# Kernel optimization log

Measured on AMD Instinct MI355X. Metric: run time of the kernel, lower is better.

## Reference

```python
import jax, jax.numpy as jnp
import numpy as np

N_WAY = 64
EPS = 1e-5  # torch LayerNorm default


def _layernorm(x, g, b):
    mu = jnp.mean(x, axis=-1, keepdims=True)
    var = jnp.mean(jnp.square(x - mu), axis=-1, keepdims=True)
    return (x - mu) * jax.lax.rsqrt(var + EPS) * g + b


def _backbone(x, params):
    (W1, b1, g1, be1, W2, b2, g2, be2, W3, b3, g3, be3, W4, b4) = params
    h = jax.nn.relu(_layernorm(x @ W1.T + b1, g1, be1))
    h = jax.nn.relu(_layernorm(h @ W2.T + b2, g2, be2))
    h = jax.nn.relu(_layernorm(h @ W3.T + b3, g3, be3))
    return h @ W4.T + b4


def setup_inputs() -> dict:
    key = jax.random.key(0)
    ks = jax.random.split(key, 20)
    d = {}
    d["support_features"] = jax.random.normal(ks[0], (32768, 768), jnp.float32)
    d["support_labels"] = jax.random.randint(ks[1], (32768,), 0, N_WAY, jnp.int64)
    d["query_features"] = jax.random.normal(ks[2], (65536, 768), jnp.float32)
    dims = [(512, 768), (512, 512), (128, 512), (32, 128)]
    ki = 3
    for i, (dout, din) in enumerate(dims, start=1):
        scale = 1.0 / np.sqrt(din)
        d[f"W{i}"] = jax.random.uniform(ks[ki], (dout, din), jnp.float32, -scale, scale); ki += 1
        d[f"b{i}"] = jax.random.uniform(ks[ki], (dout,), jnp.float32, -scale, scale); ki += 1
        if i < 4:
            d[f"g{i}"] = jnp.ones((dout,), jnp.float32)
            d[f"be{i}"] = jnp.zeros((dout,), jnp.float32)
    return d


def reference(support_features, support_labels, query_features,
              W1, b1, g1, be1, W2, b2, g2, be2, W3, b3, g3, be3, W4, b4):
    params = (W1, b1, g1, be1, W2, b2, g2, be2, W3, b3, g3, be3, W4, b4)
    z_support = _backbone(support_features, params)   # [Ns, 32]
    z_query = _backbone(query_features, params)       # [Nq, 32]
    # segment-mean prototypes (replaces per-class nonzero+mean loop)
    sums = jax.ops.segment_sum(z_support, support_labels, num_segments=N_WAY)
    counts = jax.ops.segment_sum(jnp.ones((z_support.shape[0],), z_support.dtype),
                                 support_labels, num_segments=N_WAY)
    z_proto = sums / jnp.maximum(counts, 1.0)[:, None]  # [n_way, 32]
    # -cdist (euclidean)
    sq = (jnp.sum(z_query * z_query, axis=1)[:, None]
          + jnp.sum(z_proto * z_proto, axis=1)[None, :]
          - 2.0 * z_query @ z_proto.T)
    return -jnp.sqrt(jnp.maximum(sq, 0.0))  # [Nq, n_way]
```

## Files before the change

kernel.cpp:

```cpp
#include <hip/hip_runtime.h>

typedef unsigned short u16;
typedef short bf16x8 __attribute__((ext_vector_type(8)));
typedef float f32x16 __attribute__((ext_vector_type(16)));
typedef unsigned short u16x4v __attribute__((ext_vector_type(4)));
typedef unsigned short u16x8v __attribute__((ext_vector_type(8)));

#define LN_EPS 1e-5f

__device__ __forceinline__ u16 f2bf(float v) {
    unsigned x = __float_as_uint(v);
    x += 0x7fffu + ((x >> 16) & 1u);
    return (u16)(x >> 16);
}
__device__ __forceinline__ float bf2f(u16 u) {
    return __uint_as_float(((unsigned)u) << 16);
}

#define GLD16(gp, lp) __builtin_amdgcn_global_load_lds( \
    (const __attribute__((address_space(1))) void*)(gp), \
    (__attribute__((address_space(3))) void*)(lp), 16, 0, 0)

__global__ __launch_bounds__(256)
void swizzle_split(const float* __restrict__ src, u16* __restrict__ hi,
                   u16* __restrict__ lo, int R, int DIN)
{
    __shared__ __align__(16) u16 SH[2][24][17][8];
    const int tid  = threadIdx.x;
    const int row0 = blockIdx.x * 16;
    const int QK   = DIN / 16;
    const int kq0  = QK * blockIdx.y;
    const int NKC  = DIN / 32;

    const int slots = 16 * QK;
    for (int s = tid; s < slots; s += 256) {
        int row = s / QK, kq = s % QK;
        float4 v = *(const float4*)(src + (long)(row0 + row) * DIN + (long)(kq0 + kq) * 4);
        int kc = kq >> 1, jh = (kq & 1) * 4;
        float vv[4] = {v.x, v.y, v.z, v.w};
        u16x4v h, l;
#pragma unroll
        for (int j = 0; j < 4; ++j) {
            u16 hb = f2bf(vv[j]);
            h[j] = hb;
            l[j] = f2bf(vv[j] - bf2f(hb));
        }
        *(u16x4v*)(&SH[0][kc][row][jh]) = h;
        *(u16x4v*)(&SH[1][kc][row][jh]) = l;
    }
    __syncthreads();
    const int chunks = NKC * 16;
    for (int s = tid; s < chunks; s += 256) {
        int row = s & 15, kc = s >> 4;
        long o = ((long)(kq0 / 2 + kc) * R + row0 + row) * 8;
        *(u16x8v*)(hi + o) = *(const u16x8v*)(&SH[0][kc][row][0]);
        *(u16x8v*)(lo + o) = *(const u16x8v*)(&SH[1][kc][row][0]);
    }
}

template<int DOUT, bool OUT_SPLIT, int NT>
__device__ __forceinline__ void ln_epilogue(
    f32x16 (&acc)[2][NT], float (&lnp)[4][64][2],
    const float* __restrict__ bias, const float* __restrict__ gam,
    const float* __restrict__ bet,
    u16* __restrict__ Yh, u16* __restrict__ Yl, float* __restrict__ Yf,
    long row0, int NR, int wv, int l31, int hh)
{
    float gg[NT], bb[NT], bev[NT];
#pragma unroll
    for (int u = 0; u < NT; ++u) {
        int c = wv * (DOUT / 4) + u * 32 + l31;
        bb[u] = bias[c]; gg[u] = gam[c]; bev[u] = bet[c];
    }
#pragma unroll
    for (int t = 0; t < 2; ++t)
#pragma unroll
        for (int r = 0; r < 16; ++r) {
            float s1 = 0.f, s2 = 0.f;
#pragma unroll
            for (int u = 0; u < NT; ++u) {
                float v = acc[t][u][r] + bb[u];
                acc[t][u][r] = v;
                s1 += v; s2 += v * v;
            }
#pragma unroll
            for (int off = 1; off < 32; off <<= 1) {
                s1 += __shfl_xor(s1, off, 64);
                s2 += __shfl_xor(s2, off, 64);
            }
            int row = t * 32 + (r & 3) + 8 * (r >> 2) + 4 * hh;
            if (l31 == r) { lnp[wv][row][0] = s1; lnp[wv][row][1] = s2; }
        }
    __syncthreads();
#pragma unroll
    for (int t = 0; t < 2; ++t)
#pragma unroll
        for (int r = 0; r < 16; ++r) {
            int row = t * 32 + (r & 3) + 8 * (r >> 2) + 4 * hh;
            float s1 = lnp[0][row][0] + lnp[1][row][0] + lnp[2][row][0] + lnp[3][row][0];
            float s2 = lnp[0][row][1] + lnp[1][row][1] + lnp[2][row][1] + lnp[3][row][1];
            float mean = s1 * (1.f / DOUT);
            float inv  = rsqrtf(s2 * (1.f / DOUT) - mean * mean + LN_EPS);
            long gr = row0 + row;
#pragma unroll
            for (int u = 0; u < NT; ++u) {
                int c = wv * (DOUT / 4) + u * 32 + l31;
                float v = (acc[t][u][r] - mean) * inv * gg[u] + bev[u];
                v = fmaxf(v, 0.f);
                if (OUT_SPLIT) {
                    u16 hv = f2bf(v);
                    long o = ((long)(c >> 3) * NR + gr) * 8 + (c & 7);
                    Yh[o] = hv;
                    Yl[o] = f2bf(v - bf2f(hv));
                } else {
                    Yf[gr * DOUT + c] = v;
                }
            }
        }
}

template<int DOUT>
__global__ __launch_bounds__(256, 2)
void mfma_layer1(const float* __restrict__ X,
                 const u16* __restrict__ Wh, const u16* __restrict__ Wl,
                 const float* __restrict__ bias, const float* __restrict__ gam,
                 const float* __restrict__ bet,
                 u16* __restrict__ Yh, u16* __restrict__ Yl,
                 int DIN, int NR, long rbase)
{
    constexpr int NT = DOUT / 128;
    __shared__ __align__(16) u16 AL[2][4][2][2][520];
    __shared__ float lnp[4][64][2];

    const int tid  = threadIdx.x;
    const int lane = tid & 63, wv = tid >> 6;
    const int l31  = lane & 31, hh = lane >> 5;
    const long lrow0 = (long)blockIdx.x * 64;
    const long row0  = rbase + lrow0;

    const int srow  = wv * 16 + (lane >> 2);
    const int kpart = lane & 3;
    const float* xp = X + (lrow0 + srow) * DIN + kpart * 16;

    f32x16 acc[2][NT];
#pragma unroll
    for (int t = 0; t < 2; ++t)
#pragma unroll
        for (int u = 0; u < NT; ++u)
#pragma unroll
            for (int e = 0; e < 16; ++e) acc[t][u][e] = 0.f;

    const int nslab = DIN / 64;

    auto stage = [&](const float* p, int buf) {
#pragma unroll
        for (int c = 0; c < 2; ++c) {
            float4 v0 = *(const float4*)(p + c * 8);
            float4 v1 = *(const float4*)(p + c * 8 + 4);
            float f[8] = {v0.x, v0.y, v0.z, v0.w, v1.x, v1.y, v1.z, v1.w};
            u16x8v h, l;
#pragma unroll
            for (int j = 0; j < 8; ++j) {
                u16 hb = f2bf(f[j]);
                h[j] = hb;
                l[j] = f2bf(f[j] - bf2f(hb));
            }
            *(u16x8v*)(&AL[buf][kpart][0][c][srow * 8]) = h;
            *(u16x8v*)(&AL[buf][kpart][1][c][srow * 8]) = l;
        }
    };

    stage(xp, 0);
    for (int sl = 0; sl < nslab; ++sl) {
        __syncthreads();
        const int cb = sl & 1;
        if (sl + 1 < nslab) stage(xp + (sl + 1) * 64, cb ^ 1);
#pragma unroll
        for (int s = 0; s < 4; ++s) {
            const int ks = sl * 4 + s;
            bf16x8 wf[NT][2], af[2][2];
#pragma unroll
            for (int u = 0; u < NT; ++u) {
                long wo = ((long)(2 * ks + hh) * DOUT + wv * (DOUT / 4) + u * 32 + l31) * 8;
                wf[u][0] = *(const bf16x8*)(Wh + wo);
                wf[u][1] = *(const bf16x8*)(Wl + wo);
            }
#pragma unroll
            for (int t = 0; t < 2; ++t) {
                af[t][0] = *(const bf16x8*)(&AL[cb][s][0][hh][(t * 32 + l31) * 8]);
                af[t][1] = *(const bf16x8*)(&AL[cb][s][1][hh][(t * 32 + l31) * 8]);
            }
#pragma unroll
            for (int t = 0; t < 2; ++t)
#pragma unroll
                for (int u = 0; u < NT; ++u) {
                    acc[t][u] = __builtin_amdgcn_mfma_f32_32x32x16_bf16(af[t][0], wf[u][0], acc[t][u], 0, 0, 0);
                    acc[t][u] = __builtin_amdgcn_mfma_f32_32x32x16_bf16(af[t][0], wf[u][1], acc[t][u], 0, 0, 0);
                    acc[t][u] = __builtin_amdgcn_mfma_f32_32x32x16_bf16(af[t][1], wf[u][0], acc[t][u], 0, 0, 0);
                }
        }
    }

    ln_epilogue<DOUT, true, NT>(acc, lnp, bias, gam, bet, Yh, Yl, nullptr,
                                row0, NR, wv, l31, hh);
}

template<int DOUT, bool OUT_SPLIT>
__global__ __launch_bounds__(256, 2)
void mfma_layer(const u16* __restrict__ Ah, const u16* __restrict__ Al,
                const u16* __restrict__ Wh, const u16* __restrict__ Wl,
                const float* __restrict__ bias, const float* __restrict__ gam,
                const float* __restrict__ bet,
                u16* __restrict__ Yh, u16* __restrict__ Yl,
                float* __restrict__ Yf, int DIN, int NR)
{
    constexpr int NT = DOUT / 128;
    __shared__ __align__(16) u16 AL[2][4][2][2][64 * 8];
    __shared__ float lnp[4][64][2];

    const int tid  = threadIdx.x;
    const int lane = tid & 63, wv = tid >> 6;
    const int l31  = lane & 31, hh = lane >> 5;
    const long row0 = (long)blockIdx.x * 64;

    const u16* gpA[4];
    const long stA = (long)8 * NR * 8;
#pragma unroll
    for (int t = 0; t < 4; ++t) {
        int p = t & 1, c = t >> 1;
        const u16* base = p ? Al : Ah;
        gpA[t] = base + ((long)(2 * wv + c) * NR + row0 + lane) * 8;
    }

    f32x16 acc[2][NT];
#pragma unroll
    for (int t = 0; t < 2; ++t)
#pragma unroll
        for (int u = 0; u < NT; ++u)
#pragma unroll
            for (int e = 0; e < 16; ++e) acc[t][u][e] = 0.f;

    const int nslab = DIN / 64;
#pragma unroll
    for (int t = 0; t < 4; ++t) {
        GLD16(gpA[t], &AL[0][wv][t & 1][t >> 1][0]);
        gpA[t] += stA;
    }

    for (int sl = 0; sl < nslab; ++sl) {
        __syncthreads();
        const int cb = sl & 1;
        if (sl + 1 < nslab) {
#pragma unroll
            for (int t = 0; t < 4; ++t) {
                GLD16(gpA[t], &AL[cb ^ 1][wv][t & 1][t >> 1][0]);
                gpA[t] += stA;
            }
        }
#pragma unroll
        for (int s = 0; s < 4; ++s) {
            const int ks = sl * 4 + s;
            bf16x8 wf[NT][2], af[2][2];
#pragma unroll
            for (int u = 0; u < NT; ++u) {
                long wo = ((long)(2 * ks + hh) * DOUT + wv * (DOUT / 4) + u * 32 + l31) * 8;
                wf[u][0] = *(const bf16x8*)(Wh + wo);
                wf[u][1] = *(const bf16x8*)(Wl + wo);
            }
#pragma unroll
            for (int t = 0; t < 2; ++t) {
                af[t][0] = *(const bf16x8*)(&AL[cb][s][0][hh][(t * 32 + l31) * 8]);
                af[t][1] = *(const bf16x8*)(&AL[cb][s][1][hh][(t * 32 + l31) * 8]);
            }
#pragma unroll
            for (int t = 0; t < 2; ++t)
#pragma unroll
                for (int u = 0; u < NT; ++u) {
                    acc[t][u] = __builtin_amdgcn_mfma_f32_32x32x16_bf16(af[t][0], wf[u][0], acc[t][u], 0, 0, 0);
                    acc[t][u] = __builtin_amdgcn_mfma_f32_32x32x16_bf16(af[t][0], wf[u][1], acc[t][u], 0, 0, 0);
                    acc[t][u] = __builtin_amdgcn_mfma_f32_32x32x16_bf16(af[t][1], wf[u][0], acc[t][u], 0, 0, 0);
                }
        }
    }

    ln_epilogue<DOUT, OUT_SPLIT, NT>(acc, lnp, bias, gam, bet, Yh, Yl, Yf,
                                     row0, NR, wv, l31, hh);
}

__global__ __launch_bounds__(256)
void layer4_k(const float* __restrict__ H, const float* __restrict__ W4,
              const float* __restrict__ b4, float* __restrict__ Z)
{
    __shared__ float Ws[32 * 128];
    __shared__ float bs[32];
    const int tid = threadIdx.x;
    for (int idx = tid; idx < 4096; idx += 256) Ws[idx] = W4[idx];
    if (tid < 32) bs[tid] = b4[tid];
    __syncthreads();

    long r = (long)blockIdx.x * 256 + tid;
    float acc[32];
#pragma unroll
    for (int c = 0; c < 32; ++c) acc[c] = 0.f;
    for (int k = 0; k < 128; k += 4) {
        float4 x = *(const float4*)(H + r * 128 + k);
#pragma unroll
        for (int c = 0; c < 32; ++c) {
            acc[c] = fmaf(x.x, Ws[c * 128 + k + 0], acc[c]);
            acc[c] = fmaf(x.y, Ws[c * 128 + k + 1], acc[c]);
            acc[c] = fmaf(x.z, Ws[c * 128 + k + 2], acc[c]);
            acc[c] = fmaf(x.w, Ws[c * 128 + k + 3], acc[c]);
        }
    }
#pragma unroll
    for (int c = 0; c < 32; ++c) Z[r * 32 + c] = acc[c] + bs[c];
}

__global__ __launch_bounds__(256)
void proto_k(const float* __restrict__ Zs, const int* __restrict__ lab,
             float* __restrict__ P)
{
    const int c = blockIdx.x;
    const int tid = threadIdx.x, lane = tid & 63, wv = tid >> 6;
    float acc[32];
#pragma unroll
    for (int d = 0; d < 32; ++d) acc[d] = 0.f;
    float cnt = 0.f;
    for (int i = tid; i < 32768; i += 256) {
        if (lab[i] == c) {
            cnt += 1.f;
#pragma unroll
            for (int d = 0; d < 32; ++d) acc[d] += Zs[(long)i * 32 + d];
        }
    }
    __shared__ float wsum[4][32];
    __shared__ float wcnt[4];
#pragma unroll
    for (int d = 0; d < 32; ++d) {
        float v = acc[d];
        for (int off = 32; off > 0; off >>= 1) v += __shfl_xor(v, off, 64);
        if (lane == 0) wsum[wv][d] = v;
    }
    {
        float v = cnt;
        for (int off = 32; off > 0; off >>= 1) v += __shfl_xor(v, off, 64);
        if (lane == 0) wcnt[wv] = v;
    }
    __syncthreads();
    if (tid < 32) {
        float s  = wsum[0][tid] + wsum[1][tid] + wsum[2][tid] + wsum[3][tid];
        float cn = wcnt[0] + wcnt[1] + wcnt[2] + wcnt[3];
        P[c * 32 + tid] = s / fmaxf(cn, 1.f);
    }
}

__global__ __launch_bounds__(256)
void dist_k(const float* __restrict__ Zq, const float* __restrict__ P,
            float* __restrict__ O)
{
    __shared__ float ps[64 * 32];
    __shared__ float pn[64];
    const int tid = threadIdx.x;
    for (int idx = tid; idx < 2048; idx += 256) ps[idx] = P[idx];
    __syncthreads();
    if (tid < 64) {
        float s = 0.f;
        for (int d = 0; d < 32; ++d) { float v = ps[tid * 32 + d]; s += v * v; }
        pn[tid] = s;
    }
    __syncthreads();

    long q = (long)blockIdx.x * 256 + tid;
    float zr[32];
#pragma unroll
    for (int d = 0; d < 32; d += 4) {
        float4 v = *(const float4*)(Zq + q * 32 + d);
        zr[d] = v.x; zr[d + 1] = v.y; zr[d + 2] = v.z; zr[d + 3] = v.w;
    }
    float zz = 0.f;
#pragma unroll
    for (int d = 0; d < 32; ++d) zz += zr[d] * zr[d];
    for (int p = 0; p < 64; ++p) {
        float dot = 0.f;
#pragma unroll
        for (int d = 0; d < 32; ++d) dot = fmaf(zr[d], ps[p * 32 + d], dot);
        float sq = zz + pn[p] - 2.f * dot;
        O[q * 64 + p] = -sqrtf(fmaxf(sq, 0.f));
    }
}

extern "C" void kernel_launch(void* const* d_in, const int* in_sizes, int n_in,
                              void* d_out, int out_size, void* d_ws, size_t ws_size,
                              hipStream_t stream)
{
    const float* supp = (const float*)d_in[0];
    const int*   lab  = (const int*)  d_in[1];
    const float* qry  = (const float*)d_in[2];
    const float* W1 = (const float*)d_in[3];  const float* b1 = (const float*)d_in[4];
    const float* g1 = (const float*)d_in[5];  const float* be1= (const float*)d_in[6];
    const float* W2 = (const float*)d_in[7];  const float* b2 = (const float*)d_in[8];
    const float* g2 = (const float*)d_in[9];  const float* be2= (const float*)d_in[10];
    const float* W3 = (const float*)d_in[11]; const float* b3 = (const float*)d_in[12];
    const float* g3 = (const float*)d_in[13]; const float* be3= (const float*)d_in[14];
    const float* W4 = (const float*)d_in[15]; const float* b4 = (const float*)d_in[16];
    float* out = (float*)d_out;

    const long NTOT = 98304, NS = 32768, NQ = 65536;
    const int  NR = (int)NTOT;

    char* wsp = (char*)d_ws;
    size_t off = 0;
    auto take = [&](size_t bytes) {
        char* p = wsp + off;
        off += (bytes + 255) & ~(size_t)255;
        return (void*)p;
    };

    float* zAll  = (float*)take((size_t)NTOT * 32 * 4);
    float* proto = (float*)take(2048 * 4);
    u16* W1h = (u16*)take((size_t)512 * 768 * 2);
    u16* W1l = (u16*)take((size_t)512 * 768 * 2);
    u16* W2h = (u16*)take((size_t)512 * 512 * 2);
    u16* W2l = (u16*)take((size_t)512 * 512 * 2);
    u16* W3h = (u16*)take((size_t)128 * 512 * 2);
    u16* W3l = (u16*)take((size_t)128 * 512 * 2);
    u16* h1h = (u16*)take((size_t)NTOT * 512 * 2);
    u16* h1l = (u16*)take((size_t)NTOT * 512 * 2);
    u16* h2h = (u16*)take((size_t)NTOT * 512 * 2);
    u16* h2l = (u16*)take((size_t)NTOT * 512 * 2);
    float* h3 = (float*)take((size_t)NTOT * 128 * 4);

    swizzle_split<<<dim3(32, 4), dim3(256), 0, stream>>>(W1, W1h, W1l, 512, 768);
    swizzle_split<<<dim3(32, 4), dim3(256), 0, stream>>>(W2, W2h, W2l, 512, 512);
    swizzle_split<<<dim3(8, 4),  dim3(256), 0, stream>>>(W3, W3h, W3l, 128, 512);

    mfma_layer1<512><<<dim3(NS / 64), dim3(256), 0, stream>>>(
        supp, W1h, W1l, b1, g1, be1, h1h, h1l, 768, NR, 0);
    mfma_layer1<512><<<dim3(NQ / 64), dim3(256), 0, stream>>>(
        qry, W1h, W1l, b1, g1, be1, h1h, h1l, 768, NR, NS);

    mfma_layer<512, true><<<dim3(NTOT / 64), dim3(256), 0, stream>>>(
        h1h, h1l, W2h, W2l, b2, g2, be2, h2h, h2l, nullptr, 512, NR);
    mfma_layer<128, false><<<dim3(NTOT / 64), dim3(256), 0, stream>>>(
        h2h, h2l, W3h, W3l, b3, g3, be3, nullptr, nullptr, h3, 512, NR);
    layer4_k<<<dim3(NTOT / 256), dim3(256), 0, stream>>>(h3, W4, b4, zAll);

    proto_k<<<dim3(64),  dim3(256), 0, stream>>>(zAll, lab, proto);
    dist_k<<<dim3(256), dim3(256), 0, stream>>>(zAll + NS * 32, proto, out);
}
```

Baseline: 1.011 ms.

## Stream A operands directly from global into registers, dropping LDS staging

The MFMA layer kernels stop staging activation tiles through double-buffered shared memory with block barriers. Each wave now loads its own A fragments (and, in layer 1, converts fp32 input to bf16 hi/lo pairs in registers) straight from global memory every k-step. This removes LDS traffic and __syncthreads. The cost is that each of the four waves reloads the same A rows, which raises global/L2 traffic and exposes load latency without explicit prefetch.

After: 1.123 ms. +11.0%, slower.

```diff
diff --git a/kernel.cpp b/kernel.cpp
--- a/kernel.cpp
+++ b/kernel.cpp
@@ -16,10 +16,6 @@
 __device__ __forceinline__ float bf2f(u16 u) {
     return __uint_as_float(((unsigned)u) << 16);
 }
-
-#define GLD16(gp, lp) __builtin_amdgcn_global_load_lds( \
-    (const __attribute__((address_space(1))) void*)(gp), \
-    (__attribute__((address_space(3))) void*)(lp), 16, 0, 0)
 
 __global__ __launch_bounds__(256)
 void swizzle_split(const float* __restrict__ src, u16* __restrict__ hi,
@@ -119,17 +115,88 @@
         }
 }
 
-template<int DOUT>
+template<int DOUT, bool OUT_SPLIT>
 __global__ __launch_bounds__(256, 2)
-void mfma_layer1(const float* __restrict__ X,
+void mfma_stream(const u16* __restrict__ Ah, const u16* __restrict__ Al,
                  const u16* __restrict__ Wh, const u16* __restrict__ Wl,
                  const float* __restrict__ bias, const float* __restrict__ gam,
                  const float* __restrict__ bet,
                  u16* __restrict__ Yh, u16* __restrict__ Yl,
-                 int DIN, int NR, long rbase)
+                 float* __restrict__ Yf, int DIN, int NR)
 {
     constexpr int NT = DOUT / 128;
-    __shared__ __align__(16) u16 AL[2][4][2][2][520];
+    __shared__ float lnp[4][64][2];
+
+    const int tid  = threadIdx.x;
+    const int lane = tid & 63, wv = tid >> 6;
+    const int l31  = lane & 31, hh = lane >> 5;
+    const long row0 = (long)blockIdx.x * 64;
+
+    const u16* pA[2][2];
+#pragma unroll
+    for (int t = 0; t < 2; ++t) {
+        long o = ((long)hh * NR + row0 + t * 32 + l31) * 8;
+        pA[t][0] = Ah + o;
+        pA[t][1] = Al + o;
+    }
+    const u16* pW[NT][2];
+#pragma unroll
+    for (int u = 0; u < NT; ++u) {
+        long o = ((long)hh * DOUT + wv * (DOUT / 4) + u * 32 + l31) * 8;
+        pW[u][0] = Wh + o;
+        pW[u][1] = Wl + o;
+    }
+    const long sA = (long)2 * NR * 8;
+    const long sW = (long)2 * DOUT * 8;
+
+    f32x16 acc[2][NT];
+#pragma unroll
+    for (int t = 0; t < 2; ++t)
+#pragma unroll
+        for (int u = 0; u < NT; ++u)
+#pragma unroll
+            for (int e = 0; e < 16; ++e) acc[t][u][e] = 0.f;
+
+    for (int ks = 0; ks < DIN / 16; ++ks) {
+        bf16x8 af[2][2], wf[NT][2];
+#pragma unroll
+        for (int t = 0; t < 2; ++t)
+#pragma unroll
+            for (int p = 0; p < 2; ++p) {
+                af[t][p] = *(const bf16x8*)pA[t][p];
+                pA[t][p] += sA;
+            }
+#pragma unroll
+        for (int u = 0; u < NT; ++u)
+#pragma unroll
+            for (int p = 0; p < 2; ++p) {
+                wf[u][p] = *(const bf16x8*)pW[u][p];
+                pW[u][p] += sW;
+            }
+#pragma unroll
+        for (int t = 0; t < 2; ++t)
+#pragma unroll
+            for (int u = 0; u < NT; ++u) {
+                acc[t][u] = __builtin_amdgcn_mfma_f32_32x32x16_bf16(af[t][0], wf[u][0], acc[t][u], 0, 0, 0);
+                acc[t][u] = __builtin_amdgcn_mfma_f32_32x32x16_bf16(af[t][0], wf[u][1], acc[t][u], 0, 0, 0);
+                acc[t][u] = __builtin_amdgcn_mfma_f32_32x32x16_bf16(af[t][1], wf[u][0], acc[t][u], 0, 0, 0);
+            }
+    }
+
+    ln_epilogue<DOUT, OUT_SPLIT, NT>(acc, lnp, bias, gam, bet, Yh, Yl, Yf,
+                                     row0, NR, wv, l31, hh);
+}
+
+template<int DOUT>
+__global__ __launch_bounds__(256, 2)
+void mfma_stream1(const float* __restrict__ X,
+                  const u16* __restrict__ Wh, const u16* __restrict__ Wl,
+                  const float* __restrict__ bias, const float* __restrict__ gam,
+                  const float* __restrict__ bet,
+                  u16* __restrict__ Yh, u16* __restrict__ Yl,
+                  int DIN, int NR, long rbase)
+{
+    constexpr int NT = DOUT / 128;
     __shared__ float lnp[4][64][2];
 
     const int tid  = threadIdx.x;
@@ -138,9 +205,19 @@
     const long lrow0 = (long)blockIdx.x * 64;
     const long row0  = rbase + lrow0;
 
-    const int srow  = wv * 16 + (lane >> 2);
-    const int kpart = lane & 3;
-    const float* xp = X + (lrow0 + srow) * DIN + kpart * 16;
+    const float* pX[2];
+#pragma unroll
+    for (int t = 0; t < 2; ++t)
+        pX[t] = X + (lrow0 + t * 32 + l31) * DIN + hh * 8;
+
+    const u16* pW[NT][2];
+#pragma unroll
+    for (int u = 0; u < NT; ++u) {
+        long o = ((long)hh * DOUT + wv * (DOUT / 4) + u * 32 + l31) * 8;
+        pW[u][0] = Wh + o;
+        pW[u][1] = Wl + o;
+    }
+    const long sW = (long)2 * DOUT * 8;
 
     f32x16 acc[2][NT];
 #pragma unroll
@@ -150,13 +227,13 @@
 #pragma unroll
             for (int e = 0; e < 16; ++e) acc[t][u][e] = 0.f;
 
-    const int nslab = DIN / 64;
-
-    auto stage = [&](const float* p, int buf) {
-#pragma unroll
-        for (int c = 0; c < 2; ++c) {
-            float4 v0 = *(const float4*)(p + c * 8);
-            float4 v1 = *(const float4*)(p + c * 8 + 4);
+    for (int ks = 0; ks < DIN / 16; ++ks) {
+        bf16x8 af[2][2], wf[NT][2];
+#pragma unroll
+        for (int t = 0; t < 2; ++t) {
+            float4 v0 = *(const float4*)pX[t];
+            float4 v1 = *(const float4*)(pX[t] + 4);
+            pX[t] += 16;
             float f[8] = {v0.x, v0.y, v0.z, v0.w, v1.x, v1.y, v1.z, v1.w};
             u16x8v h, l;
 #pragma unroll
@@ -165,126 +242,28 @@
                 h[j] = hb;
                 l[j] = f2bf(f[j] - bf2f(hb));
             }
-            *(u16x8v*)(&AL[buf][kpart][0][c][srow * 8]) = h;
-            *(u16x8v*)(&AL[buf][kpart][1][c][srow * 8]) = l;
-        }
-    };
-
-    stage(xp, 0);
-    for (int sl = 0; sl < nslab; ++sl) {
-        __syncthreads();
-        const int cb = sl & 1;
-        if (sl + 1 < nslab) stage(xp + (sl + 1) * 64, cb ^ 1);
-#pragma unroll
-        for (int s = 0; s < 4; ++s) {
-            const int ks = sl * 4 + s;
-            bf16x8 wf[NT][2], af[2][2];
+            af[t][0] = *(bf16x8*)&h;
+            af[t][1] = *(bf16x8*)&l;
+        }
+#pragma unroll
+        for (int u = 0; u < NT; ++u)
+#pragma unroll
+            for (int p = 0; p < 2; ++p) {
+                wf[u][p] = *(const bf16x8*)pW[u][p];
+                pW[u][p] += sW;
+            }
+#pragma unroll
+        for (int t = 0; t < 2; ++t)
 #pragma unroll
             for (int u = 0; u < NT; ++u) {
-                long wo = ((long)(2 * ks + hh) * DOUT + wv * (DOUT / 4) + u * 32 + l31) * 8;
-                wf[u][0] = *(const bf16x8*)(Wh + wo);
-                wf[u][1] = *(const bf16x8*)(Wl + wo);
-            }
-#pragma unroll
-            for (int t = 0; t < 2; ++t) {
-                af[t][0] = *(const bf16x8*)(&AL[cb][s][0][hh][(t * 32 + l31) * 8]);
-                af[t][1] = *(const bf16x8*)(&AL[cb][s][1][hh][(t * 32 + l31) * 8]);
-            }
-#pragma unroll
-            for (int t = 0; t < 2; ++t)
-#pragma unroll
-                for (int u = 0; u < NT; ++u) {
-                    acc[t][u] = __builtin_amdgcn_mfma_f32_32x32x16_bf16(af[t][0], wf[u][0], acc[t][u], 0, 0, 0);
-                    acc[t][u] = __builtin_amdgcn_mfma_f32_32x32x16_bf16(af[t][0], wf[u][1], acc[t][u], 0, 0, 0);
-                    acc[t][u] = __builtin_amdgcn_mfma_f32_32x32x16_bf16(af[t][1], wf[u][0], acc[t][u], 0, 0, 0);
-                }
-        }
+                acc[t][u] = __builtin_amdgcn_mfma_f32_32x32x16_bf16(af[t][0], wf[u][0], acc[t][u], 0, 0, 0);
+                acc[t][u] = __builtin_amdgcn_mfma_f32_32x32x16_bf16(af[t][0], wf[u][1], acc[t][u], 0, 0, 0);
+                acc[t][u] = __builtin_amdgcn_mfma_f32_32x32x16_bf16(af[t][1], wf[u][0], acc[t][u], 0, 0, 0);
+            }
     }
 
     ln_epilogue<DOUT, true, NT>(acc, lnp, bias, gam, bet, Yh, Yl, nullptr,
                                 row0, NR, wv, l31, hh);
-}
-
-template<int DOUT, bool OUT_SPLIT>
-__global__ __launch_bounds__(256, 2)
-void mfma_layer(const u16* __restrict__ Ah, const u16* __restrict__ Al,
-                const u16* __restrict__ Wh, const u16* __restrict__ Wl,
-                const float* __restrict__ bias, const float* __restrict__ gam,
-                const float* __restrict__ bet,
-                u16* __restrict__ Yh, u16* __restrict__ Yl,
-                float* __restrict__ Yf, int DIN, int NR)
-{
-    constexpr int NT = DOUT / 128;
-    __shared__ __align__(16) u16 AL[2][4][2][2][64 * 8];
-    __shared__ float lnp[4][64][2];
-
-    const int tid  = threadIdx.x;
-    const int lane = tid & 63, wv = tid >> 6;
-    const int l31  = lane & 31, hh = lane >> 5;
-    const long row0 = (long)blockIdx.x * 64;
-
-    const u16* gpA[4];
-    const long stA = (long)8 * NR * 8;
-#pragma unroll
-    for (int t = 0; t < 4; ++t) {
-        int p = t & 1, c = t >> 1;
-        const u16* base = p ? Al : Ah;
-        gpA[t] = base + ((long)(2 * wv + c) * NR + row0 + lane) * 8;
-    }
-
-    f32x16 acc[2][NT];
-#pragma unroll
-    for (int t = 0; t < 2; ++t)
-#pragma unroll
-        for (int u = 0; u < NT; ++u)
-#pragma unroll
-            for (int e = 0; e < 16; ++e) acc[t][u][e] = 0.f;
-
-    const int nslab = DIN / 64;
-#pragma unroll
-    for (int t = 0; t < 4; ++t) {
-        GLD16(gpA[t], &AL[0][wv][t & 1][t >> 1][0]);
-        gpA[t] += stA;
-    }
-
-    for (int sl = 0; sl < nslab; ++sl) {
-        __syncthreads();
-        const int cb = sl & 1;
-        if (sl + 1 < nslab) {
-#pragma unroll
-            for (int t = 0; t < 4; ++t) {
-                GLD16(gpA[t], &AL[cb ^ 1][wv][t & 1][t >> 1][0]);
-                gpA[t] += stA;
-            }
-        }
-#pragma unroll
-        for (int s = 0; s < 4; ++s) {
-            const int ks = sl * 4 + s;
-            bf16x8 wf[NT][2], af[2][2];
-#pragma unroll
-            for (int u = 0; u < NT; ++u) {
-                long wo = ((long)(2 * ks + hh) * DOUT + wv * (DOUT / 4) + u * 32 + l31) * 8;
-                wf[u][0] = *(const bf16x8*)(Wh + wo);
-                wf[u][1] = *(const bf16x8*)(Wl + wo);
-            }
-#pragma unroll
-            for (int t = 0; t < 2; ++t) {
-                af[t][0] = *(const bf16x8*)(&AL[cb][s][0][hh][(t * 32 + l31) * 8]);
-                af[t][1] = *(const bf16x8*)(&AL[cb][s][1][hh][(t * 32 + l31) * 8]);
-            }
-#pragma unroll
-            for (int t = 0; t < 2; ++t)
-#pragma unroll
-                for (int u = 0; u < NT; ++u) {
-                    acc[t][u] = __builtin_amdgcn_mfma_f32_32x32x16_bf16(af[t][0], wf[u][0], acc[t][u], 0, 0, 0);
-                    acc[t][u] = __builtin_amdgcn_mfma_f32_32x32x16_bf16(af[t][0], wf[u][1], acc[t][u], 0, 0, 0);
-                    acc[t][u] = __builtin_amdgcn_mfma_f32_32x32x16_bf16(af[t][1], wf[u][0], acc[t][u], 0, 0, 0);
-                }
-        }
-    }
-
-    ln_epilogue<DOUT, OUT_SPLIT, NT>(acc, lnp, bias, gam, bet, Yh, Yl, Yf,
-                                     row0, NR, wv, l31, hh);
 }
 
 __global__ __launch_bounds__(256)
@@ -434,14 +413,14 @@
     swizzle_split<<<dim3(32, 4), dim3(256), 0, stream>>>(W2, W2h, W2l, 512, 512);
     swizzle_split<<<dim3(8, 4),  dim3(256), 0, stream>>>(W3, W3h, W3l, 128, 512);
 
-    mfma_layer1<512><<<dim3(NS / 64), dim3(256), 0, stream>>>(
+    mfma_stream1<512><<<dim3(NS / 64), dim3(256), 0, stream>>>(
         supp, W1h, W1l, b1, g1, be1, h1h, h1l, 768, NR, 0);
-    mfma_layer1<512><<<dim3(NQ / 64), dim3(256), 0, stream>>>(
+    mfma_stream1<512><<<dim3(NQ / 64), dim3(256), 0, stream>>>(
         qry, W1h, W1l, b1, g1, be1, h1h, h1l, 768, NR, NS);
 
-    mfma_layer<512, true><<<dim3(NTOT / 64), dim3(256), 0, stream>>>(
+    mfma_stream<512, true><<<dim3(NTOT / 64), dim3(256), 0, stream>>>(
         h1h, h1l, W2h, W2l, b2, g2, be2, h2h, h2l, nullptr, 512, NR);
-    mfma_layer<128, false><<<dim3(NTOT / 64), dim3(256), 0, stream>>>(
+    mfma_stream<128, false><<<dim3(NTOT / 64), dim3(256), 0, stream>>>(
         h2h, h2l, W3h, W3l, b3, g3, be3, nullptr, nullptr, h3, 512, NR);
     layer4_k<<<dim3(NTOT / 256), dim3(256), 0, stream>>>(h3, W4, b4, zAll);
 
```
